# Kernel optimization log

Measured on AMD Instinct MI355X. Metric: run time of the kernel, lower is better.

Reference implementation:

```python
import jax, jax.numpy as jnp
import numpy as np

B, T, I, H, C, L, N_AHEAD = 64, 512, 64, 512, 512, 2, 24


def _lstm_layer(x, w_ih, w_hh, b_ih, b_hh):
    """PyTorch-convention LSTM layer. x: [B,T,in]. Returns (outputs [B,T,H], hT, cT)."""
    bsz = x.shape[0]
    hdim = w_hh.shape[1]
    bias = b_ih + b_hh

    def step(carry, xt):
        h, c = carry
        g = xt @ w_ih.T + h @ w_hh.T + bias  # [B, 4H], gate order i,f,g,o
        i, f, gg, o = jnp.split(g, 4, axis=-1)
        c = jax.nn.sigmoid(f) * c + jax.nn.sigmoid(i) * jnp.tanh(gg)
        h = jax.nn.sigmoid(o) * jnp.tanh(c)
        return (h, c), h

    init = (jnp.zeros((bsz, hdim), x.dtype), jnp.zeros((bsz, hdim), x.dtype))
    (hT, cT), hs = jax.lax.scan(step, init, jnp.swapaxes(x, 0, 1))
    return jnp.swapaxes(hs, 0, 1), hT, cT


def setup_inputs() -> dict:
    key = jax.random.key(0)
    ks = jax.random.split(key, 16)
    s = 0.04  # ~ 1/sqrt(H) init scale
    d = {
        "x": jax.random.normal(ks[0], (B, T, I), jnp.float32),
        "w_ih0": jax.random.normal(ks[1], (4 * H, I), jnp.float32) * s,
        "w_hh0": jax.random.normal(ks[2], (4 * H, H), jnp.float32) * s,
        "b_ih0": jax.random.normal(ks[3], (4 * H,), jnp.float32) * s,
        "b_hh0": jax.random.normal(ks[4], (4 * H,), jnp.float32) * s,
        "w_ih1": jax.random.normal(ks[5], (4 * H, H), jnp.float32) * s,
        "w_hh1": jax.random.normal(ks[6], (4 * H, H), jnp.float32) * s,
        "b_ih1": jax.random.normal(ks[7], (4 * H,), jnp.float32) * s,
        "b_hh1": jax.random.normal(ks[8], (4 * H,), jnp.float32) * s,
        "w_ih_dec": jax.random.normal(ks[9], (4 * H, C), jnp.float32) * s,
        "w_hh_dec": jax.random.normal(ks[10], (4 * H, H), jnp.float32) * s,
        "b_ih_dec": jax.random.normal(ks[11], (4 * H,), jnp.float32) * s,
        "b_hh_dec": jax.random.normal(ks[12], (4 * H,), jnp.float32) * s,
        "w_fc": jax.random.normal(ks[13], (C, H), jnp.float32) * s,
        "b_fc": jax.random.normal(ks[14], (C,), jnp.float32) * s,
    }
    return d


def reference(x, w_ih0, w_hh0, b_ih0, b_hh0, w_ih1, w_hh1, b_ih1, b_hh1,
              w_ih_dec, w_hh_dec, b_ih_dec, b_hh_dec, w_fc, b_fc):
    # ---- encoder: 2-layer LSTM, batch_first ----
    h0_out, _, _ = _lstm_layer(x, w_ih0, w_hh0, b_ih0, b_hh0)
    enc, hT, cT = _lstm_layer(h0_out, w_ih1, w_hh1, b_ih1, b_hh1)  # enc: [B,T,H]

    bsz = x.shape[0]
    dec_bias = b_ih_dec + b_hh_dec
    dec_in0 = jnp.zeros((bsz, C), x.dtype)

    def dec_step(carry, _):
        h, c, dec_in = carry
        aw = jax.nn.softmax(jnp.einsum('bth,bh->bt', enc, h), axis=1)  # [B,T]
        ctx = jnp.einsum('bt,bth->bh', aw, enc)                         # [B,H]
        xi = dec_in + ctx                                               # requires C == H
        g = xi @ w_ih_dec.T + h @ w_hh_dec.T + dec_bias
        i, f, gg, o = jnp.split(g, 4, axis=-1)
        c = jax.nn.sigmoid(f) * c + jax.nn.sigmoid(i) * jnp.tanh(gg)
        h = jax.nn.sigmoid(o) * jnp.tanh(c)
        pred = h @ w_fc.T + b_fc                                        # [B,C]
        return (h, c, pred), pred

    _, preds = jax.lax.scan(dec_step, (hT, cT, dec_in0), None, length=N_AHEAD)
    return jnp.swapaxes(preds, 0, 1)  # [B, n_ahead, C]
```

## Files before the change

kernel.cpp:

```cpp
#include <hip/hip_runtime.h>

#define BATCH  64
#define TT     512
#define IDIM   64
#define HDIM   512
#define NAHEAD 24
#define HB     (HDIM * BATCH)

#define WIH0_OFF   0
#define WHH0_OFF   512
#define WIH1_OFF   4608
#define WHH1_OFF   8704
#define SCR_OFF    12800
#define GL_OFF     30208
#define BIAS_OFF   31232
#define ENC_SMEM_FLOATS 31248
#define ENC_SMEM_BYTES  (ENC_SMEM_FLOATS * 4)

typedef float v2f __attribute__((ext_vector_type(2)));

__device__ __forceinline__ float4 ld4(const float* p) {
  return *reinterpret_cast<const float4*>(p);
}
__device__ __forceinline__ float sigm(float x) { return 1.0f / (1.0f + expf(-x)); }

__device__ __forceinline__ void AS(float* p, float v) {
  __hip_atomic_store(p, v, __ATOMIC_RELAXED, __HIP_MEMORY_SCOPE_AGENT);
}

__device__ __forceinline__ void flag_barrier(unsigned* flags, unsigned epoch,
                                             int bid) {
  asm volatile("s_waitcnt vmcnt(0)" ::: "memory");
  __syncthreads();
  if (threadIdx.x == 0)
    __hip_atomic_store(&flags[(size_t)bid * 16], epoch,
                       __ATOMIC_RELAXED, __HIP_MEMORY_SCOPE_AGENT);
  asm volatile("" ::: "memory");
  if (threadIdx.x < 64) {
    const int l = threadIdx.x;
    for (;;) {
      bool ok = true;
#pragma unroll
      for (int i = 0; i < 4; ++i) {
        unsigned v = __hip_atomic_load(&flags[(size_t)(l * 4 + i) * 16],
                                       __ATOMIC_RELAXED, __HIP_MEMORY_SCOPE_AGENT);
        ok &= (v >= epoch);
      }
      if (__all(ok)) break;
      __builtin_amdgcn_s_sleep(1);
    }
  }
  __syncthreads();
  asm volatile("" ::: "memory");
}

#define STG8(dst, base, off0)                                          \
  _Pragma("unroll") for (int i = 0; i < 8; ++i) {                      \
    dst[i].x = (base)[((off0) + i) * BATCH];                           \
    dst[i].y = (base)[((off0) + i) * BATCH + 32];                      \
  }

#define BURN_S(sarr, C0)                                                      \
  do {                                                                        \
    _Pragma("unroll") for (int c = 0; c < 8; c += 4) {                        \
      if (t < TT) {                                                           \
        _Pragma("unroll") for (int d = 0; d < 8; ++d) {                       \
          float4 w = ld4(&smem[WHH0_OFF + d * HDIM + ks * 16 + (C0) + c]);    \
          a0[d] += sarr[c]*w.x + sarr[c+1]*w.y + sarr[c+2]*w.z + sarr[c+3]*w.w;\
        }                                                                     \
      }                                                                       \
      if (t >= 1) {                                                           \
        _Pragma("unroll") for (int d = 0; d < 8; ++d) {                       \
          float4 w = ld4(&smem[WIH1_OFF + d * HDIM + ks * 16 + (C0) + c]);    \
          a1[d] += sarr[c]*w.x + sarr[c+1]*w.y + sarr[c+2]*w.z + sarr[c+3]*w.w;\
        }                                                                     \
      }                                                                       \
    }                                                                         \
  } while (0)

#define BURN_E(earr, C0)                                                      \
  do {                                                                        \
    if (t >= 1) {                                                             \
      _Pragma("unroll") for (int c = 0; c < 8; c += 4) {                      \
        _Pragma("unroll") for (int d = 0; d < 8; ++d) {                       \
          float4 w = ld4(&smem[WHH1_OFF + d * HDIM + ks * 16 + (C0) + c]);    \
          a1[d] += earr[c]*w.x + earr[c+1]*w.y + earr[c+2]*w.z + earr[c+3]*w.w;\
        }                                                                     \
      }                                                                       \
    }                                                                         \
  } while (0)

__global__ __launch_bounds__(1024, 4)
void encoder_coop(const float* __restrict__ xT,
                  const float* __restrict__ w_ih0, const float* __restrict__ w_hh0,
                  const float* __restrict__ b_ih0, const float* __restrict__ b_hh0,
                  const float* __restrict__ w_ih1, const float* __restrict__ w_hh1,
                  const float* __restrict__ b_ih1, const float* __restrict__ b_hh1,
                  float* __restrict__ seq0,
                  float* __restrict__ enc,
                  float* __restrict__ cst1,
                  unsigned* flags)
{
  extern __shared__ float smem[];
  const int tid  = threadIdx.x;
  const int bid  = blockIdx.x;
  const int j0   = bid * 2;
  const int lane = tid & 63;
  const int wv   = tid >> 6;
  const int bp   = tid & 31;
  const int ks   = tid >> 5;

  for (int idx = tid; idx < 8 * IDIM; idx += 1024) {
    int d = idx >> 6, k = idx & 63;
    size_t r = (size_t)((d >> 1) * HDIM + j0 + (d & 1));
    smem[WIH0_OFF + idx] = w_ih0[r * IDIM + k];
  }
  for (int idx = tid; idx < 8 * HDIM; idx += 1024) {
    int d = idx >> 9, k = idx & 511;
    size_t r = (size_t)((d >> 1) * HDIM + j0 + (d & 1));
    smem[WHH0_OFF + idx] = w_hh0[r * HDIM + k];
    smem[WIH1_OFF + idx] = w_ih1[r * HDIM + k];
    smem[WHH1_OFF + idx] = w_hh1[r * HDIM + k];
  }
  if (tid < 16) {
    int d = tid & 7;
    size_t r = (size_t)((d >> 1) * HDIM + j0 + (d & 1));
    smem[BIAS_OFF + tid] = (tid < 8) ? (b_ih0[r] + b_hh0[r])
                                     : (b_ih1[r] + b_hh1[r]);
  }
  __syncthreads();

  float c0 = 0.f;
  float c1 = 0.f;

  for (int t = 0; t <= TT; ++t) {
    const float* sp = seq0 + (size_t)t * HB + (size_t)(ks * 16) * BATCH + bp;
    const float* ep = enc + (size_t)(t >= 1 ? t - 1 : 0) * HB
                          + (size_t)(ks * 16) * BATCH + bp;

    v2f sA[8], sB[8], eA[8], eB[8];
    v2f xv[4];

    STG8(sA, sp, 0);
    STG8(sB, sp, 8);
    if (t < TT && ks < 16) {
      const float* xp = xT + (size_t)t * IDIM * BATCH
                           + (size_t)(ks * 4) * BATCH + bp;
#pragma unroll
      for (int i = 0; i < 4; ++i) {
        xv[i].x = xp[i * BATCH];
        xv[i].y = xp[i * BATCH + 32];
      }
    }

    v2f a0[8], a1[8];
#pragma unroll
    for (int d = 0; d < 8; ++d) { a0[d] = 0.f; a1[d] = 0.f; }

    if (t < TT && ks < 16) {
#pragma unroll
      for (int d = 0; d < 8; ++d) {
        float4 w = ld4(&smem[WIH0_OFF + d * IDIM + ks * 4]);
        a0[d] += xv[0]*w.x + xv[1]*w.y + xv[2]*w.z + xv[3]*w.w;
      }
    }

    BURN_S(sA, 0);
    if (t >= 1) STG8(eA, ep, 0);
    BURN_S(sB, 8);
    if (t >= 1) STG8(eB, ep, 8);
    BURN_E(eA, 0);
    BURN_E(eB, 8);

#pragma unroll
    for (int d = 0; d < 8; ++d) {
      float m0x = a0[d].x + __shfl_xor(a0[d].x, 32);
      float m0y = a0[d].y + __shfl_xor(a0[d].y, 32);
      smem[SCR_OFF + (d * 64 + lane) * 17 + wv] = (lane >= 32) ? m0y : m0x;
      float m1x = a1[d].x + __shfl_xor(a1[d].x, 32);
      float m1y = a1[d].y + __shfl_xor(a1[d].y, 32);
      smem[SCR_OFF + ((8 + d) * 64 + lane) * 17 + wv] = (lane >= 32) ? m1y : m1x;
    }
    __syncthreads();

    {
      const int dd = tid >> 6, bb = tid & 63;
      float s = 0.f;
#pragma unroll
      for (int i = 0; i < 16; ++i) s += smem[SCR_OFF + (dd * 64 + bb) * 17 + i];
      smem[GL_OFF + dd * 64 + bb] = s + smem[BIAS_OFF + dd];
    }
    __syncthreads();

    if (tid < 256) {
      const int bb = tid & 63, u = tid >> 6;
      if (u < 2) {
        if (t < TT) {
          const int cl = u;
          float gi = smem[GL_OFF + (0 + cl) * 64 + bb];
          float gf = smem[GL_OFF + (2 + cl) * 64 + bb];
          float gg = smem[GL_OFF + (4 + cl) * 64 + bb];
          float go = smem[GL_OFF + (6 + cl) * 64 + bb];
          float cn = sigm(gf) * c0 + sigm(gi) * tanhf(gg);
          float hn = sigm(go) * tanhf(cn);
          c0 = cn;
          AS(&seq0[(size_t)(t + 1) * HB + (size_t)(j0 + cl) * BATCH + bb], hn);
        }
      } else {
        if (t >= 1) {
          const int cl = u - 2;
          float gi = smem[GL_OFF + (8 + 0 + cl) * 64 + bb];
          float gf = smem[GL_OFF + (8 + 2 + cl) * 64 + bb];
          float gg = smem[GL_OFF + (8 + 4 + cl) * 64 + bb];
          float go = smem[GL_OFF + (8 + 6 + cl) * 64 + bb];
          float cn = sigm(gf) * c1 + sigm(gi) * tanhf(gg);
          float hn = sigm(go) * tanhf(cn);
          c1 = cn;
          AS(&enc[(size_t)t * HB + (size_t)(j0 + cl) * BATCH + bb], hn);
        }
      }
    }

    if (t < TT) flag_barrier(flags, (unsigned)(t + 1), bid);
  }

  if (tid >= 128 && tid < 256)
    cst1[(size_t)(j0 + ((tid >> 6) - 2)) * BATCH + (tid & 63)] = c1;
}

template <int DIN0>
__device__ __forceinline__ void cell_tile2(
    int j0, const float* __restrict__ in0,
    const float* __restrict__ h_in,
    const float* __restrict__ w_ih,
    const float* __restrict__ w_hh,
    const float* __restrict__ b_ih, const float* __restrict__ b_hh,
    float* __restrict__ c_state,
    float* __restrict__ h_out,
    float* __restrict__ sm)
{
  const int tid = threadIdx.x;
  const int b  = tid & 63;
  const int ks = tid >> 6;
  constexpr int K  = DIN0 + HDIM;
  constexpr int KS = K / 16;
  const int k0 = ks * KS, k1 = k0 + KS;
  const int a0 = (k0 < DIN0) ? k0 : DIN0;
  const int a1 = (k1 < DIN0) ? k1 : DIN0;
  const int c0 = (k0 > DIN0) ? k0 - DIN0 : 0;
  const int c1 = (k1 > DIN0) ? k1 - DIN0 : 0;

  const float* wi = w_ih + (size_t)j0 * DIN0;
  const float* wh = w_hh + (size_t)j0 * HDIM;

  float acc[8] = {0.f, 0.f, 0.f, 0.f, 0.f, 0.f, 0.f, 0.f};

#pragma unroll 2
  for (int k = a0; k < a1; k += 4) {
    float x0 = in0[(k + 0) * BATCH + b];
    float x1 = in0[(k + 1) * BATCH + b];
    float x2 = in0[(k + 2) * BATCH + b];
    float x3 = in0[(k + 3) * BATCH + b];
#pragma unroll
    for (int d = 0; d < 8; ++d) {
      float4 w = ld4(wi + (size_t)((d >> 1) * HDIM + (d & 1)) * DIN0 + k);
      acc[d] += x0 * w.x + x1 * w.y + x2 * w.z + x3 * w.w;
    }
  }
#pragma unroll 2
  for (int k = c0; k < c1; k += 4) {
    float h0 = h_in[(k + 0) * BATCH + b];
    float h1 = h_in[(k + 1) * BATCH + b];
    float h2 = h_in[(k + 2) * BATCH + b];
    float h3 = h_in[(k + 3) * BATCH + b];
#pragma unroll
    for (int d = 0; d < 8; ++d) {
      float4 w = ld4(wh + (size_t)((d >> 1) * HDIM + (d & 1)) * HDIM + k);
      acc[d] += h0 * w.x + h1 * w.y + h2 * w.z + h3 * w.w;
    }
  }

  float* gl = sm + 8 * 64 * 17;
#pragma unroll
  for (int d = 0; d < 8; ++d) sm[(d * 64 + b) * 17 + ks] = acc[d];
  __syncthreads();

  if (tid < 512) {
    const int dd = tid >> 6, bb = tid & 63;
    float s = 0.f;
#pragma unroll
    for (int i = 0; i < 16; ++i) s += sm[(dd * 64 + bb) * 17 + i];
    const int r = (dd >> 1) * HDIM + j0 + (dd & 1);
    gl[dd * 64 + bb] = s + b_ih[r] + b_hh[r];
  }
  __syncthreads();

  if (tid < 128) {
    const int bb = tid & 63, cl = tid >> 6;
    const int jc = j0 + cl;
    float gi = gl[(0 + cl) * 64 + bb];
    float gf = gl[(2 + cl) * 64 + bb];
    float gg = gl[(4 + cl) * 64 + bb];
    float go = gl[(6 + cl) * 64 + bb];
    float cold = c_state[(size_t)jc * BATCH + bb];
    float cn = sigm(gf) * cold + sigm(gi) * tanhf(gg);
    float hn = sigm(go) * tanhf(cn);
    c_state[(size_t)jc * BATCH + bb] = cn;
    h_out[(size_t)jc * BATCH + bb] = hn;
  }
  __syncthreads();
}

__global__ __launch_bounds__(1024, 1)
void lstm_step(int t,
               const float* __restrict__ xT,
               const float* __restrict__ w_ih0, const float* __restrict__ w_hh0,
               const float* __restrict__ b_ih0, const float* __restrict__ b_hh0,
               const float* __restrict__ w_ih1, const float* __restrict__ w_hh1,
               const float* __restrict__ b_ih1, const float* __restrict__ b_hh1,
               float* __restrict__ seq0, float* __restrict__ enc,
               float* __restrict__ cst0, float* __restrict__ cst1)
{
  __shared__ float sm[8 * 64 * 17 + 8 * 64];
  const int j0 = blockIdx.x * 2;
  if (t < TT)
    cell_tile2<IDIM>(j0, xT + (size_t)t * IDIM * BATCH,
                     seq0 + (size_t)t * HB,
                     w_ih0, w_hh0, b_ih0, b_hh0,
                     cst0, seq0 + (size_t)(t + 1) * HB, sm);
  if (t >= 1)
    cell_tile2<HDIM>(j0, seq0 + (size_t)t * HB,
                     enc + (size_t)(t - 1) * HB,
                     w_ih1, w_hh1, b_ih1, b_hh1,
                     cst1, enc + (size_t)t * HB, sm);
}

__global__ __launch_bounds__(1024, 1)
void dec_gates(const float* __restrict__ xi, const float* __restrict__ h_cur,
               const float* __restrict__ w_ih, const float* __restrict__ w_hh,
               const float* __restrict__ b_ih, const float* __restrict__ b_hh,
               float* __restrict__ cst, float* __restrict__ h_out)
{
  __shared__ float sm[8 * 64 * 17 + 8 * 64];
  cell_tile2<HDIM>(blockIdx.x * 2, xi, h_cur, w_ih, w_hh, b_ih, b_hh,
                   cst, h_out, sm);
}

__global__ __launch_bounds__(512, 2)
void attn_scores(const float* __restrict__ enc,
                 const float* __restrict__ h_cur,
                 float* __restrict__ scores)
{
  __shared__ float red[2][8][64];
  const int tid = threadIdx.x;
  const int b  = tid & 63;
  const int ks = tid >> 6;
  const int t0 = blockIdx.x * 2;
  const float* e0 = enc + (size_t)(t0 + 1) * HB + ks * 64 * BATCH;
  const float* e1 = e0 + HB;
  const float* hr = h_cur + ks * 64 * BATCH;
  float a0 = 0.f, a1 = 0.f;
#pragma unroll 4
  for (int k = 0; k < 64; ++k) {
    float hv = hr[k * BATCH + b];
    a0 += hv * e0[k * BATCH + b];
    a1 += hv * e1[k * BATCH + b];
  }
  red[0][ks][b] = a0;
  red[1][ks][b] = a1;
  __syncthreads();
  if (tid < 128) {
    int tl = tid >> 6;
    float s = 0.f;
#pragma unroll
    for (int i = 0; i < 8; ++i) s += red[tl][i][b];
    scores[(size_t)(t0 + tl) * BATCH + b] = s;
  }
}

__global__ __launch_bounds__(512, 2)
void attn_ctx(const float* __restrict__ enc,
              const float* __restrict__ scores,
              const float* __restrict__ h_cur,
              const float* __restrict__ w_fc, const float* __restrict__ b_fc,
              float* __restrict__ xi,
              float* __restrict__ out,
              int s)
{
  __shared__ float red[8][2][64];
  __shared__ float mz[2][64];
  __shared__ float ctxv[2][64];
  const int tid = threadIdx.x;
  const int b  = tid & 63;
  const int ts = tid >> 6;
  const int hc0 = blockIdx.x * 2;

  float m = -1e30f;
  for (int t = ts * 64; t < ts * 64 + 64; ++t)
    m = fmaxf(m, scores[(size_t)t * BATCH + b]);
  red[ts][0][b] = m;
  __syncthreads();
  if (tid < 64) {
    float mm = red[0][0][b];
#pragma unroll
    for (int i = 1; i < 8; ++i) mm = fmaxf(mm, red[i][0][b]);
    mz[0][b] = mm;
  }
  __syncthreads();
  m = mz[0][b];
  float z = 0.f;
  for (int t = ts * 64; t < ts * 64 + 64; ++t)
    z += expf(scores[(size_t)t * BATCH + b] - m);
  red[ts][1][b] = z;
  __syncthreads();
  if (tid < 64) {
    float zz = 0.f;
#pragma unroll
    for (int i = 0; i < 8; ++i) zz += red[i][1][b];
    mz[1][b] = 1.f / zz;
  }
  __syncthreads();
  const float rZ = mz[1][b];

  float a0 = 0.f, a1 = 0.f;
  const float* eb = enc + HB + (size_t)hc0 * BATCH + b;
  for (int t = ts * 64; t < ts * 64 + 64; ++t) {
    float p = expf(scores[(size_t)t * BATCH + b] - m) * rZ;
    a0 += p * eb[(size_t)t * HB];
    a1 += p * eb[(size_t)t * HB + BATCH];
  }
  __syncthreads();
  red[ts][0][b] = a0;
  red[ts][1][b] = a1;
  __syncthreads();
  if (tid < 128) {
    int cl = tid >> 6;
    float c = 0.f;
#pragma unroll
    for (int i = 0; i < 8; ++i) c += red[i][cl][b];
    ctxv[cl][b] = c;
  }

  float p0 = 0.f, p1 = 0.f;
  if (s >= 1) {
    const float* w0 = w_fc + (size_t)hc0 * HDIM + ts * 64;
    const float* w1 = w0 + HDIM;
    const float* hr = h_cur + ts * 64 * BATCH;
#pragma unroll 2
    for (int k = 0; k < 64; k += 4) {
      float4 wa = ld4(w0 + k), wb = ld4(w1 + k);
      float h0 = hr[(k + 0) * BATCH + b], h1 = hr[(k + 1) * BATCH + b];
      float h2 = hr[(k + 2) * BATCH + b], h3 = hr[(k + 3) * BATCH + b];
      p0 += wa.x * h0 + wa.y * h1 + wa.z * h2 + wa.w * h3;
      p1 += wb.x * h0 + wb.y * h1 + wb.z * h2 + wb.w * h3;
    }
  }
  __syncthreads();
  red[ts][0][b] = p0;
  red[ts][1][b] = p1;
  __syncthreads();
  if (tid < 128) {
    int cl = tid >> 6;
    int cc = hc0 + cl;
    float pred = 0.f;
    if (s >= 1) {
#pragma unroll
      for (int i = 0; i < 8; ++i) pred += red[i][cl][b];
      pred += b_fc[cc];
      out[((size_t)b * NAHEAD + (s - 1)) * HDIM + cc] = pred;
    }
    xi[(size_t)cc * BATCH + b] = ctxv[cl][b] + pred;
  }
}

__global__ __launch_bounds__(512, 2)
void fc_out(const float* __restrict__ h, const float* __restrict__ w_fc,
            const float* __restrict__ b_fc, float* __restrict__ out, int srow)
{
  __shared__ float red[8][2][64];
  const int tid = threadIdx.x;
  const int b  = tid & 63;
  const int ks = tid >> 6;
  const int cc0 = blockIdx.x * 2;
  const float* w0 = w_fc + (size_t)cc0 * HDIM + ks * 64;
  const float* w1 = w0 + HDIM;
  const float* hr = h + ks * 64 * BATCH;
  float p0 = 0.f, p1 = 0.f;
#pragma unroll 2
  for (int k = 0; k < 64; k += 4) {
    float4 wa = ld4(w0 + k), wb = ld4(w1 + k);
    float h0 = hr[(k + 0) * BATCH + b], h1 = hr[(k + 1) * BATCH + b];
    float h2 = hr[(k + 2) * BATCH + b], h3 = hr[(k + 3) * BATCH + b];
    p0 += wa.x * h0 + wa.y * h1 + wa.z * h2 + wa.w * h3;
    p1 += wb.x * h0 + wb.y * h1 + wb.z * h2 + wb.w * h3;
  }
  red[ks][0][b] = p0;
  red[ks][1][b] = p1;
  __syncthreads();
  if (tid < 128) {
    int cl = tid >> 6;
    int cc = cc0 + cl;
    float p = 0.f;
#pragma unroll
    for (int i = 0; i < 8; ++i) p += red[i][cl][b];
    out[((size_t)b * NAHEAD + srow) * HDIM + cc] = p + b_fc[cc];
  }
}

__global__ __launch_bounds__(256)
void transpose_x(const float* __restrict__ x, float* __restrict__ xT)
{
  __shared__ float tile[64][65];
  const int t = blockIdx.x;
  const int lane = threadIdx.x & 63;
  const int w    = threadIdx.x >> 6;
#pragma unroll
  for (int ii = 0; ii < 16; ++ii) {
    int b = w * 16 + ii;
    tile[b][lane] = x[((size_t)b * TT + t) * IDIM + lane];
  }
  __syncthreads();
#pragma unroll
  for (int ii = 0; ii < 16; ++ii) {
    int i = w * 16 + ii;
    xT[((size_t)t * IDIM + i) * BATCH + lane] = tile[lane][i];
  }
}

extern "C" void kernel_launch(void* const* d_in, const int* in_sizes, int n_in,
                              void* d_out, int out_size, void* d_ws, size_t ws_size,
                              hipStream_t stream) {
  const float* x     = (const float*)d_in[0];
  const float* w_ih0 = (const float*)d_in[1];
  const float* w_hh0 = (const float*)d_in[2];
  const float* b_ih0 = (const float*)d_in[3];
  const float* b_hh0 = (const float*)d_in[4];
  const float* w_ih1 = (const float*)d_in[5];
  const float* w_hh1 = (const float*)d_in[6];
  const float* b_ih1 = (const float*)d_in[7];
  const float* b_hh1 = (const float*)d_in[8];
  const float* w_ihd = (const float*)d_in[9];
  const float* w_hhd = (const float*)d_in[10];
  const float* b_ihd = (const float*)d_in[11];
  const float* b_hhd = (const float*)d_in[12];
  const float* w_fc  = (const float*)d_in[13];
  const float* b_fc  = (const float*)d_in[14];
  float* out = (float*)d_out;

  char* ws = (char*)d_ws;
  size_t off = 0;
  auto alloc = [&](size_t bytes) -> void* {
    void* p = ws + off;
    off += (bytes + 255) & ~(size_t)255;
    return p;
  };

  float* cst0 = (float*)alloc((size_t)HB * 4);
  float* cst1 = (float*)alloc((size_t)HB * 4);
  float* seq0 = (float*)alloc((size_t)(TT + 1) * HB * 4);
  float* enc  = (float*)alloc((size_t)(TT + 1) * HB * 4);
  float* xT   = (float*)alloc((size_t)TT * IDIM * BATCH * 4);
  float* scores = (float*)alloc((size_t)TT * BATCH * 4);
  float* xi     = (float*)alloc((size_t)HB * 4);
  float* hdec   = (float*)alloc((size_t)2 * HB * 4);
  unsigned* flags   = (unsigned*)alloc(256 * 16 * 4);
  (void)ws_size; (void)in_sizes; (void)n_in; (void)out_size;

  hipMemsetAsync(cst0, 0, (size_t)HB * 4 * 2, stream);
  hipMemsetAsync(seq0, 0, (size_t)HB * 4, stream);
  hipMemsetAsync(enc,  0, (size_t)HB * 4, stream);
  hipMemsetAsync(flags, 0, 256 * 16 * 4, stream);

  transpose_x<<<TT, 256, 0, stream>>>(x, xT);

  static bool attr_set = false;
  if (!attr_set) {
    hipFuncSetAttribute(reinterpret_cast<const void*>(encoder_coop),
                        hipFuncAttributeMaxDynamicSharedMemorySize,
                        ENC_SMEM_BYTES);
    attr_set = true;
  }

  void* args[] = {
    (void*)&xT,
    (void*)&w_ih0, (void*)&w_hh0, (void*)&b_ih0, (void*)&b_hh0,
    (void*)&w_ih1, (void*)&w_hh1, (void*)&b_ih1, (void*)&b_hh1,
    (void*)&seq0, (void*)&enc, (void*)&cst1, (void*)&flags
  };
  hipError_t cerr = hipLaunchCooperativeKernel(
      reinterpret_cast<void*>(encoder_coop), dim3(256), dim3(1024),
      args, (unsigned)ENC_SMEM_BYTES, stream);
  if (cerr != hipSuccess) {
    for (int t = 0; t <= TT; ++t) {
      lstm_step<<<256, 1024, 0, stream>>>(
          t, xT, w_ih0, w_hh0, b_ih0, b_hh0,
          w_ih1, w_hh1, b_ih1, b_hh1, seq0, enc, cst0, cst1);
    }
  }

  const float* h_cur = enc + (size_t)TT * HB;
  for (int s = 0; s < NAHEAD; ++s) {
    attn_scores<<<256, 512, 0, stream>>>(enc, h_cur, scores);
    attn_ctx<<<256, 512, 0, stream>>>(enc, scores, h_cur, w_fc, b_fc,
                                      xi, out, s);
    float* h_nxt = hdec + (size_t)(s & 1) * HB;
    dec_gates<<<256, 1024, 0, stream>>>(xi, h_cur, w_ihd, w_hhd,
                                        b_ihd, b_hhd, cst1, h_nxt);
    h_cur = h_nxt;
  }
  fc_out<<<256, 512, 0, stream>>>(h_cur, w_fc, b_fc, out, NAHEAD - 1);
}
```

Before: 7.266 ms.

## Read encoder weights from global memory via scalar loads instead of LDS

Drops the LDS copy of the per-block weight slices and reads them straight from global memory on each step. Wave-uniform addresses (readfirstlane) let the compiler issue scalar loads, which are broadcast to every lane. The thread mapping changes so each lane owns one batch element and each wave owns a 32-wide k-slice, which removes the cross-half shuffle reductions. The LDS footprint shrinks a lot, but each timestep now depends on scalar cache and L2 bandwidth and latency for the weights.

```diff
diff --git a/kernel.cpp b/kernel.cpp
--- a/kernel.cpp
+++ b/kernel.cpp
@@ -7,17 +7,11 @@
 #define NAHEAD 24
 #define HB     (HDIM * BATCH)
 
-#define WIH0_OFF   0
-#define WHH0_OFF   512
-#define WIH1_OFF   4608
-#define WHH1_OFF   8704
-#define SCR_OFF    12800
-#define GL_OFF     30208
-#define BIAS_OFF   31232
-#define ENC_SMEM_FLOATS 31248
+#define SCR_OFF    0
+#define GL_OFF     17408
+#define BIAS_OFF   18432
+#define ENC_SMEM_FLOATS 18448
 #define ENC_SMEM_BYTES  (ENC_SMEM_FLOATS * 4)
-
-typedef float v2f __attribute__((ext_vector_type(2)));
 
 __device__ __forceinline__ float4 ld4(const float* p) {
   return *reinterpret_cast<const float4*>(p);
@@ -54,39 +48,40 @@
   asm volatile("" ::: "memory");
 }
 
-#define STG8(dst, base, off0)                                          \
-  _Pragma("unroll") for (int i = 0; i < 8; ++i) {                      \
-    dst[i].x = (base)[((off0) + i) * BATCH];                           \
-    dst[i].y = (base)[((off0) + i) * BATCH + 32];                      \
-  }
-
-#define BURN_S(sarr, C0)                                                      \
+#define LD8(dst, base, off0)                                           \
+  _Pragma("unroll") for (int i = 0; i < 8; ++i)                        \
+    dst[i] = (base)[((off0) + i) * BATCH];
+
+#define WROW_H(mat, d) \
+  ((mat) + (size_t)((((d) >> 1) * HDIM) + j0 + ((d) & 1)) * HDIM)
+
+#define BURN_SEQ(v, C0)                                                       \
   do {                                                                        \
-    _Pragma("unroll") for (int c = 0; c < 8; c += 4) {                        \
-      if (t < TT) {                                                           \
-        _Pragma("unroll") for (int d = 0; d < 8; ++d) {                       \
-          float4 w = ld4(&smem[WHH0_OFF + d * HDIM + ks * 16 + (C0) + c]);    \
-          a0[d] += sarr[c]*w.x + sarr[c+1]*w.y + sarr[c+2]*w.z + sarr[c+3]*w.w;\
-        }                                                                     \
+    if (t < TT) {                                                             \
+      _Pragma("unroll") for (int d = 0; d < 8; ++d) {                         \
+        const float* wp = WROW_H(w_hh0, d) + kbs + (C0);                      \
+        float4 wa = ld4(wp), wb = ld4(wp + 4);                                \
+        a0[d] += v[0]*wa.x + v[1]*wa.y + v[2]*wa.z + v[3]*wa.w                \
+               + v[4]*wb.x + v[5]*wb.y + v[6]*wb.z + v[7]*wb.w;               \
       }                                                                       \
-      if (t >= 1) {                                                           \
-        _Pragma("unroll") for (int d = 0; d < 8; ++d) {                       \
-          float4 w = ld4(&smem[WIH1_OFF + d * HDIM + ks * 16 + (C0) + c]);    \
-          a1[d] += sarr[c]*w.x + sarr[c+1]*w.y + sarr[c+2]*w.z + sarr[c+3]*w.w;\
-        }                                                                     \
+    }                                                                         \
+    if (t >= 1) {                                                             \
+      _Pragma("unroll") for (int d = 0; d < 8; ++d) {                         \
+        const float* wp = WROW_H(w_ih1, d) + kbs + (C0);                      \
+        float4 wa = ld4(wp), wb = ld4(wp + 4);                                \
+        a1[d] += v[0]*wa.x + v[1]*wa.y + v[2]*wa.z + v[3]*wa.w                \
+               + v[4]*wb.x + v[5]*wb.y + v[6]*wb.z + v[7]*wb.w;               \
       }                                                                       \
     }                                                                         \
   } while (0)
 
-#define BURN_E(earr, C0)                                                      \
+#define BURN_ENC(v, C0)                                                       \
   do {                                                                        \
-    if (t >= 1) {                                                             \
-      _Pragma("unroll") for (int c = 0; c < 8; c += 4) {                      \
-        _Pragma("unroll") for (int d = 0; d < 8; ++d) {                       \
-          float4 w = ld4(&smem[WHH1_OFF + d * HDIM + ks * 16 + (C0) + c]);    \
-          a1[d] += earr[c]*w.x + earr[c+1]*w.y + earr[c+2]*w.z + earr[c+3]*w.w;\
-        }                                                                     \
-      }                                                                       \
+    _Pragma("unroll") for (int d = 0; d < 8; ++d) {                           \
+      const float* wp = WROW_H(w_hh1, d) + kbs + (C0);                        \
+      float4 wa = ld4(wp), wb = ld4(wp + 4);                                  \
+      a1[d] += v[0]*wa.x + v[1]*wa.y + v[2]*wa.z + v[3]*wa.w                  \
+             + v[4]*wb.x + v[5]*wb.y + v[6]*wb.z + v[7]*wb.w;                 \
     }                                                                         \
   } while (0)
 
@@ -102,26 +97,14 @@
                   unsigned* flags)
 {
   extern __shared__ float smem[];
-  const int tid  = threadIdx.x;
-  const int bid  = blockIdx.x;
-  const int j0   = bid * 2;
-  const int lane = tid & 63;
-  const int wv   = tid >> 6;
-  const int bp   = tid & 31;
-  const int ks   = tid >> 5;
-
-  for (int idx = tid; idx < 8 * IDIM; idx += 1024) {
-    int d = idx >> 6, k = idx & 63;
-    size_t r = (size_t)((d >> 1) * HDIM + j0 + (d & 1));
-    smem[WIH0_OFF + idx] = w_ih0[r * IDIM + k];
-  }
-  for (int idx = tid; idx < 8 * HDIM; idx += 1024) {
-    int d = idx >> 9, k = idx & 511;
-    size_t r = (size_t)((d >> 1) * HDIM + j0 + (d & 1));
-    smem[WHH0_OFF + idx] = w_hh0[r * HDIM + k];
-    smem[WIH1_OFF + idx] = w_ih1[r * HDIM + k];
-    smem[WHH1_OFF + idx] = w_hh1[r * HDIM + k];
-  }
+  const int tid = threadIdx.x;
+  const int bid = blockIdx.x;
+  const int j0  = bid * 2;
+  const int b   = tid & 63;
+  const int wv  = tid >> 6;
+  const int wvu = __builtin_amdgcn_readfirstlane(wv);
+  const int kbs = wvu * 32;
+
   if (tid < 16) {
     int d = tid & 7;
     size_t r = (size_t)((d >> 1) * HDIM + j0 + (d & 1));
@@ -134,53 +117,54 @@
   float c1 = 0.f;
 
   for (int t = 0; t <= TT; ++t) {
-    const float* sp = seq0 + (size_t)t * HB + (size_t)(ks * 16) * BATCH + bp;
+    const float* sp = seq0 + (size_t)t * HB + (size_t)kbs * BATCH + b;
     const float* ep = enc + (size_t)(t >= 1 ? t - 1 : 0) * HB
-                          + (size_t)(ks * 16) * BATCH + bp;
-
-    v2f sA[8], sB[8], eA[8], eB[8];
-    v2f xv[4];
-
-    STG8(sA, sp, 0);
-    STG8(sB, sp, 8);
-    if (t < TT && ks < 16) {
+                          + (size_t)kbs * BATCH + b;
+
+    float a0[8], a1[8];
+#pragma unroll
+    for (int d = 0; d < 8; ++d) { a0[d] = 0.f; a1[d] = 0.f; }
+
+    float vA[8], vB[8];
+    LD8(vA, sp, 0);
+    LD8(vB, sp, 8);
+
+    if (t < TT) {
       const float* xp = xT + (size_t)t * IDIM * BATCH
-                           + (size_t)(ks * 4) * BATCH + bp;
-#pragma unroll
-      for (int i = 0; i < 4; ++i) {
-        xv[i].x = xp[i * BATCH];
-        xv[i].y = xp[i * BATCH + 32];
+                           + (size_t)(wvu * 4) * BATCH + b;
+      float x0 = xp[0], x1 = xp[BATCH], x2 = xp[2 * BATCH], x3 = xp[3 * BATCH];
+#pragma unroll
+      for (int d = 0; d < 8; ++d) {
+        const float* wp = w_ih0 +
+            (size_t)(((d >> 1) * HDIM) + j0 + (d & 1)) * IDIM + wvu * 4;
+        float4 w = ld4(wp);
+        a0[d] += x0 * w.x + x1 * w.y + x2 * w.z + x3 * w.w;
       }
     }
 
-    v2f a0[8], a1[8];
-#pragma unroll
-    for (int d = 0; d < 8; ++d) { a0[d] = 0.f; a1[d] = 0.f; }
-
-    if (t < TT && ks < 16) {
-#pragma unroll
-      for (int d = 0; d < 8; ++d) {
-        float4 w = ld4(&smem[WIH0_OFF + d * IDIM + ks * 4]);
-        a0[d] += xv[0]*w.x + xv[1]*w.y + xv[2]*w.z + xv[3]*w.w;
-      }
-    }
-
-    BURN_S(sA, 0);
-    if (t >= 1) STG8(eA, ep, 0);
-    BURN_S(sB, 8);
-    if (t >= 1) STG8(eB, ep, 8);
-    BURN_E(eA, 0);
-    BURN_E(eB, 8);
-
-#pragma unroll
-    for (int d = 0; d < 8; ++d) {
-      float m0x = a0[d].x + __shfl_xor(a0[d].x, 32);
-      float m0y = a0[d].y + __shfl_xor(a0[d].y, 32);
-      smem[SCR_OFF + (d * 64 + lane) * 17 + wv] = (lane >= 32) ? m0y : m0x;
-      float m1x = a1[d].x + __shfl_xor(a1[d].x, 32);
-      float m1y = a1[d].y + __shfl_xor(a1[d].y, 32);
-      smem[SCR_OFF + ((8 + d) * 64 + lane) * 17 + wv] = (lane >= 32) ? m1y : m1x;
-    }
+    BURN_SEQ(vA, 0);
+    LD8(vA, sp, 16);
+    BURN_SEQ(vB, 8);
+    LD8(vB, sp, 24);
+    BURN_SEQ(vA, 16);
+    if (t >= 1) LD8(vA, ep, 0);
+    BURN_SEQ(vB, 24);
+    if (t >= 1) {
+      LD8(vB, ep, 8);
+      BURN_ENC(vA, 0);
+      LD8(vA, ep, 16);
+      BURN_ENC(vB, 8);
+      LD8(vB, ep, 24);
+      BURN_ENC(vA, 16);
+      BURN_ENC(vB, 24);
+    }
+
+#pragma unroll
+    for (int d = 0; d < 8; ++d)
+      smem[SCR_OFF + (d * 64 + b) * 17 + wv] = a0[d];
+#pragma unroll
+    for (int d = 0; d < 8; ++d)
+      smem[SCR_OFF + ((8 + d) * 64 + b) * 17 + wv] = a1[d];
     __syncthreads();
 
     {
```

Result: slower. 8.521 ms (+17.3%).
